# Performance work log

Hardware: AMD Instinct MI355X
Metric: run time of the kernel (lower is better)

Reference implementation:

```python
import jax, jax.numpy as jnp
import numpy as np

B = 65536
IN = 64
H = 128
OUT = 2


def setup_inputs() -> dict:
    key = jax.random.key(0)
    ks = jax.random.split(key, 16)
    s_in = 1.0 / np.sqrt(IN)
    s_h = 1.0 / np.sqrt(H)
    d = {}
    d["x"] = jax.random.normal(ks[0], (B, IN), dtype=jnp.float32)
    # initial state (module resets to zeros per day)
    d["h0"] = jnp.zeros((H,), dtype=jnp.float32)
    d["c0"] = jnp.zeros((B, H), dtype=jnp.float32)
    # input->hidden linears (with bias), torch Linear layout [out, in]
    for i, name in enumerate(["f", "i", "o", "c"]):
        d[f"Wx{name}"] = jax.random.uniform(ks[1 + i], (H, IN), jnp.float32, -s_in, s_in)
        d[f"bx{name}"] = jax.random.uniform(ks[5 + i], (H,), jnp.float32, -s_in, s_in)
        d[f"Wh{name}"] = jax.random.uniform(ks[9 + i], (H, H), jnp.float32, -s_h, s_h)
    d["Wy"] = jax.random.uniform(ks[13], (OUT, H), jnp.float32, -s_h, s_h)
    d["by"] = jax.random.uniform(ks[14], (OUT,), jnp.float32, -s_h, s_h)
    return d


def reference(x, h0, c0, Wxf, bxf, Wxi, bxi, Wxo, bxo, Wxc, bxc, Whf, Whi, Who, Whc, Wy, by):
    # hidden recurrent contributions (h0 is a length-H vector, broadcast over batch)
    hi = h0 @ Whi.T  # [H]
    hf = h0 @ Whf.T
    ho = h0 @ Who.T
    hc = h0 @ Whc.T
    i = jax.nn.sigmoid(x @ Wxi.T + bxi + hi)  # [B, H]
    f = jax.nn.sigmoid(x @ Wxf.T + bxf + hf)
    o = jax.nn.sigmoid(x @ Wxo.T + bxo + ho)
    c_til = jnp.tanh(x @ Wxc.T + bxc + hc)
    c = f * c0 + i * c_til
    h = o * jnp.tanh(c)
    y_hat = h @ Wy.T + by  # [B, OUT]
    return y_hat
```

## Files before the change

### kernel.cpp

```cpp
#include <hip/hip_runtime.h>


#define B_SIZE 65536

typedef __bf16 bf16x8 __attribute__((ext_vector_type(8)));
typedef __bf16 bf16x4 __attribute__((ext_vector_type(4)));
typedef float f32x4 __attribute__((ext_vector_type(4)));

__device__ __forceinline__ float fsig(float x) {
    float e = __builtin_amdgcn_exp2f(-1.442695040888963f * x);
    return __builtin_amdgcn_rcpf(1.0f + e);
}
__device__ __forceinline__ float ftanh(float x) {
    float e = __builtin_amdgcn_exp2f(2.885390081777927f * x);
    return 1.0f - 2.0f * __builtin_amdgcn_rcpf(e + 1.0f);
}

__global__ void bias_kernel(const float* __restrict__ h0,
                            const float* __restrict__ Whf, const float* __restrict__ Whi,
                            const float* __restrict__ Who, const float* __restrict__ Whc,
                            const float* __restrict__ bxf, const float* __restrict__ bxi,
                            const float* __restrict__ bxo, const float* __restrict__ bxc,
                            float* __restrict__ bias512) {
    int j = blockIdx.x * 64 + threadIdx.x;
    int g = j >> 7, r = j & 127;
    const float* Wh = (g == 0) ? Whf : (g == 1) ? Whi : (g == 2) ? Who : Whc;
    const float* bx = (g == 0) ? bxf : (g == 1) ? bxi : (g == 2) ? bxo : bxc;
    float s = bx[r];
    const float4* row = (const float4*)(Wh + r * 128);
    const float4* h4  = (const float4*)h0;
#pragma unroll 8
    for (int k = 0; k < 32; ++k) {
        float4 a = row[k], b = h4[k];
        s += a.x * b.x + a.y * b.y + a.z * b.z + a.w * b.w;
    }
    bias512[j] = s;
}

__launch_bounds__(256, 2)
__global__ void lstm_kernel(const float* __restrict__ x, const float* __restrict__ c0,
                            const float* __restrict__ Wxf, const float* __restrict__ Wxi,
                            const float* __restrict__ Wxo, const float* __restrict__ Wxc,
                            const float* __restrict__ Wy, const float* __restrict__ by,
                            const float* __restrict__ bias512, float* __restrict__ out) {
    __shared__ __bf16 xs[2][1024];
    __shared__ float cs[2][16 * 132];
    __shared__ float yred[4][64][2];

    const int tid  = threadIdx.x;
    const int lane = tid & 63;
    const int w    = tid >> 6;
    const int q    = lane >> 4;
    const int n15  = lane & 15;

    const float* Wxg[4] = {Wxf, Wxi, Wxo, Wxc};
    bf16x8 bw[4][2][2];
    float biasv[4][2];
#pragma unroll
    for (int g = 0; g < 4; ++g) {
#pragma unroll
        for (int cb = 0; cb < 2; ++cb) {
            const int n = w * 32 + cb * 16 + n15;
            biasv[g][cb] = bias512[g * 128 + n];
#pragma unroll
            for (int kb = 0; kb < 2; ++kb) {
                const float* p = Wxg[g] + n * 64 + kb * 32 + q * 8;
                float4 lo = *(const float4*)p;
                float4 hi = *(const float4*)(p + 4);
                bf16x8 v;
                v[0] = (__bf16)lo.x; v[1] = (__bf16)lo.y; v[2] = (__bf16)lo.z; v[3] = (__bf16)lo.w;
                v[4] = (__bf16)hi.x; v[5] = (__bf16)hi.y; v[6] = (__bf16)hi.z; v[7] = (__bf16)hi.w;
                bw[g][cb][kb] = v;
            }
        }
    }
    float wyv[2][2];
#pragma unroll
    for (int o = 0; o < 2; ++o)
#pragma unroll
        for (int cb = 0; cb < 2; ++cb)
            wyv[o][cb] = Wy[o * 128 + w * 32 + cb * 16 + n15];
    const float by0 = by[0], by1 = by[1];

    constexpr int ITERS = (B_SIZE / 16) / 1024;
    const int tile0 = blockIdx.x * ITERS;

    const int xrow = tid >> 4;
    const int k4   = (tid & 15) * 4;
    const int sidx = (k4 >> 5) * 512 + ((k4 & 31) >> 3) * 128 + xrow * 8 + (k4 & 7);

    const int ccol = (tid & 15) * 8;
    const int cidx = xrow * 132 + ccol;

    float4 xr  = *(const float4*)(x  + (size_t)(tile0 * 16 + xrow) * 64 + k4);
    float4 cpa = *(const float4*)(c0 + (size_t)(tile0 * 16 + xrow) * 128 + ccol);
    float4 cpb = *(const float4*)(c0 + (size_t)(tile0 * 16 + xrow) * 128 + ccol + 4);
    {
        bf16x4 v; v[0] = (__bf16)xr.x; v[1] = (__bf16)xr.y; v[2] = (__bf16)xr.z; v[3] = (__bf16)xr.w;
        *(bf16x4*)&xs[0][sidx] = v;
        *(float4*)&cs[0][cidx] = cpa;
        *(float4*)&cs[0][cidx + 4] = cpb;
    }
    xr  = *(const float4*)(x  + (size_t)((tile0 + 1) * 16 + xrow) * 64 + k4);
    cpa = *(const float4*)(c0 + (size_t)((tile0 + 1) * 16 + xrow) * 128 + ccol);
    cpb = *(const float4*)(c0 + (size_t)((tile0 + 1) * 16 + xrow) * 128 + ccol + 4);
    __syncthreads();

#pragma unroll
    for (int it = 0; it < ITERS; ++it) {
        const int cur = it & 1;

        bf16x8 a0 = *(const bf16x8*)&xs[cur][lane * 8];
        bf16x8 a1 = *(const bf16x8*)&xs[cur][512 + lane * 8];

        float c0v[2][4];
#pragma unroll
        for (int cb = 0; cb < 2; ++cb)
#pragma unroll
            for (int r = 0; r < 4; ++r)
                c0v[cb][r] = cs[cur][(q * 4 + r) * 132 + w * 32 + cb * 16 + n15];

        if (it + 1 < ITERS) {
            bf16x4 v; v[0] = (__bf16)xr.x; v[1] = (__bf16)xr.y; v[2] = (__bf16)xr.z; v[3] = (__bf16)xr.w;
            *(bf16x4*)&xs[cur ^ 1][sidx] = v;
            *(float4*)&cs[cur ^ 1][cidx] = cpa;
            *(float4*)&cs[cur ^ 1][cidx + 4] = cpb;
            if (it + 2 < ITERS) {
                const int tn = tile0 + it + 2;
                xr  = *(const float4*)(x  + (size_t)(tn * 16 + xrow) * 64 + k4);
                cpa = *(const float4*)(c0 + (size_t)(tn * 16 + xrow) * 128 + ccol);
                cpb = *(const float4*)(c0 + (size_t)(tn * 16 + xrow) * 128 + ccol + 4);
            }
        }

        f32x4 acc[4][2];
#pragma unroll
        for (int g = 0; g < 4; ++g)
#pragma unroll
            for (int cb = 0; cb < 2; ++cb) {
                float b = biasv[g][cb];
                f32x4 t = {b, b, b, b};
                acc[g][cb] = t;
            }
#pragma unroll
        for (int g = 0; g < 4; ++g)
#pragma unroll
            for (int cb = 0; cb < 2; ++cb) {
                acc[g][cb] = __builtin_amdgcn_mfma_f32_16x16x32_bf16(a0, bw[g][cb][0], acc[g][cb], 0, 0, 0);
                acc[g][cb] = __builtin_amdgcn_mfma_f32_16x16x32_bf16(a1, bw[g][cb][1], acc[g][cb], 0, 0, 0);
            }

        float p0[4] = {0.f, 0.f, 0.f, 0.f};
        float p1[4] = {0.f, 0.f, 0.f, 0.f};
#pragma unroll
        for (int cb = 0; cb < 2; ++cb)
#pragma unroll
            for (int r = 0; r < 4; ++r) {
                float fg = fsig(acc[0][cb][r]);
                float ig = fsig(acc[1][cb][r]);
                float og = fsig(acc[2][cb][r]);
                float ct = ftanh(acc[3][cb][r]);
                float c  = fg * c0v[cb][r] + ig * ct;
                float h  = og * ftanh(c);
                p0[r] += h * wyv[0][cb];
                p1[r] += h * wyv[1][cb];
            }
#pragma unroll
        for (int m = 1; m < 16; m <<= 1) {
#pragma unroll
            for (int r = 0; r < 4; ++r) {
                p0[r] += __shfl_xor(p0[r], m, 64);
                p1[r] += __shfl_xor(p1[r], m, 64);
            }
        }
        if (n15 == 0) {
#pragma unroll
            for (int r = 0; r < 4; ++r) {
                yred[w][it * 16 + q * 4 + r][0] = p0[r];
                yred[w][it * 16 + q * 4 + r][1] = p1[r];
            }
        }
        __syncthreads();
    }

    if (tid < 64) {
        float s0 = by0 + yred[0][tid][0] + yred[1][tid][0] + yred[2][tid][0] + yred[3][tid][0];
        float s1 = by1 + yred[0][tid][1] + yred[1][tid][1] + yred[2][tid][1] + yred[3][tid][1];
        float2 s = {s0, s1};
        *(float2*)(out + (size_t)(tile0 * 16 + tid) * 2) = s;
    }
}

extern "C" void kernel_launch(void* const* d_in, const int* in_sizes, int n_in,
                              void* d_out, int out_size, void* d_ws, size_t ws_size,
                              hipStream_t stream) {
    const float* x   = (const float*)d_in[0];
    const float* h0  = (const float*)d_in[1];
    const float* c0  = (const float*)d_in[2];
    const float* Wxf = (const float*)d_in[3];
    const float* bxf = (const float*)d_in[4];
    const float* Whf = (const float*)d_in[5];
    const float* Wxi = (const float*)d_in[6];
    const float* bxi = (const float*)d_in[7];
    const float* Whi = (const float*)d_in[8];
    const float* Wxo = (const float*)d_in[9];
    const float* bxo = (const float*)d_in[10];
    const float* Who = (const float*)d_in[11];
    const float* Wxc = (const float*)d_in[12];
    const float* bxc = (const float*)d_in[13];
    const float* Whc = (const float*)d_in[14];
    const float* Wy  = (const float*)d_in[15];
    const float* by  = (const float*)d_in[16];
    float* out = (float*)d_out;
    float* bias512 = (float*)d_ws;

    bias_kernel<<<8, 64, 0, stream>>>(h0, Whf, Whi, Who, Whc, bxf, bxi, bxo, bxc, bias512);
    lstm_kernel<<<1024, 256, 0, stream>>>(x, c0, Wxf, Wxi, Wxo, Wxc, Wy, by, bias512, out);
}
```

Baseline: 136.0 us.

## Pre-pack bf16 weight fragments once and halve grid to amortize per-block setup

Adds a prep kernel that converts the four input weight matrices to bf16 MFMA fragment layout once, so each LSTM block loads ready fragments with one vector load instead of two fp32 loads plus conversion. The grid is halved to 512 blocks with 8 tiles each, amortizing weight and bias setup over more batch rows. The cost is an extra kernel launch and fewer blocks in flight, which may reduce latency hiding on a 256-CU device.

```diff
diff --git a/kernel.cpp b/kernel.cpp
--- a/kernel.cpp
+++ b/kernel.cpp
@@ -37,15 +37,34 @@
     bias512[j] = s;
 }
 
+__global__ void prep_kernel(const float* __restrict__ Wxf, const float* __restrict__ Wxi,
+                            const float* __restrict__ Wxo, const float* __restrict__ Wxc,
+                            __bf16* __restrict__ frags) {
+    int t = blockIdx.x * 64 + threadIdx.x;
+    int w    = t >> 10;
+    int g    = (t >> 8) & 3;
+    int cb   = (t >> 7) & 1;
+    int kb   = (t >> 6) & 1;
+    int lane = t & 63;
+    const float* Wx = (g == 0) ? Wxf : (g == 1) ? Wxi : (g == 2) ? Wxo : Wxc;
+    const int n = w * 32 + cb * 16 + (lane & 15);
+    const float* p = Wx + n * 64 + kb * 32 + (lane >> 4) * 8;
+    float4 lo = *(const float4*)p;
+    float4 hi = *(const float4*)(p + 4);
+    bf16x8 v;
+    v[0] = (__bf16)lo.x; v[1] = (__bf16)lo.y; v[2] = (__bf16)lo.z; v[3] = (__bf16)lo.w;
+    v[4] = (__bf16)hi.x; v[5] = (__bf16)hi.y; v[6] = (__bf16)hi.z; v[7] = (__bf16)hi.w;
+    *(bf16x8*)(frags + (size_t)t * 8) = v;
+}
+
 __launch_bounds__(256, 2)
 __global__ void lstm_kernel(const float* __restrict__ x, const float* __restrict__ c0,
-                            const float* __restrict__ Wxf, const float* __restrict__ Wxi,
-                            const float* __restrict__ Wxo, const float* __restrict__ Wxc,
+                            const __bf16* __restrict__ frags,
                             const float* __restrict__ Wy, const float* __restrict__ by,
                             const float* __restrict__ bias512, float* __restrict__ out) {
     __shared__ __bf16 xs[2][1024];
     __shared__ float cs[2][16 * 132];
-    __shared__ float yred[4][64][2];
+    __shared__ float yred[4][128][2];
 
     const int tid  = threadIdx.x;
     const int lane = tid & 63;
@@ -53,27 +72,18 @@
     const int q    = lane >> 4;
     const int n15  = lane & 15;
 
-    const float* Wxg[4] = {Wxf, Wxi, Wxo, Wxc};
     bf16x8 bw[4][2][2];
     float biasv[4][2];
 #pragma unroll
-    for (int g = 0; g < 4; ++g) {
+    for (int g = 0; g < 4; ++g)
 #pragma unroll
         for (int cb = 0; cb < 2; ++cb) {
-            const int n = w * 32 + cb * 16 + n15;
-            biasv[g][cb] = bias512[g * 128 + n];
-#pragma unroll
-            for (int kb = 0; kb < 2; ++kb) {
-                const float* p = Wxg[g] + n * 64 + kb * 32 + q * 8;
-                float4 lo = *(const float4*)p;
-                float4 hi = *(const float4*)(p + 4);
-                bf16x8 v;
-                v[0] = (__bf16)lo.x; v[1] = (__bf16)lo.y; v[2] = (__bf16)lo.z; v[3] = (__bf16)lo.w;
-                v[4] = (__bf16)hi.x; v[5] = (__bf16)hi.y; v[6] = (__bf16)hi.z; v[7] = (__bf16)hi.w;
-                bw[g][cb][kb] = v;
-            }
-        }
-    }
+            biasv[g][cb] = bias512[g * 128 + w * 32 + cb * 16 + n15];
+#pragma unroll
+            for (int kb = 0; kb < 2; ++kb)
+                bw[g][cb][kb] = *(const bf16x8*)(frags +
+                    (size_t)(((w * 16 + g * 4 + cb * 2 + kb) * 64 + lane)) * 8);
+        }
     float wyv[2][2];
 #pragma unroll
     for (int o = 0; o < 2; ++o)
@@ -82,7 +92,7 @@
             wyv[o][cb] = Wy[o * 128 + w * 32 + cb * 16 + n15];
     const float by0 = by[0], by1 = by[1];
 
-    constexpr int ITERS = (B_SIZE / 16) / 1024;
+    constexpr int ITERS = (B_SIZE / 16) / 512;
     const int tile0 = blockIdx.x * ITERS;
 
     const int xrow = tid >> 4;
@@ -183,7 +193,7 @@
         __syncthreads();
     }
 
-    if (tid < 64) {
+    if (tid < 128) {
         float s0 = by0 + yred[0][tid][0] + yred[1][tid][0] + yred[2][tid][0] + yred[3][tid][0];
         float s1 = by1 + yred[0][tid][1] + yred[1][tid][1] + yred[2][tid][1] + yred[3][tid][1];
         float2 s = {s0, s1};
@@ -213,7 +223,9 @@
     const float* by  = (const float*)d_in[16];
     float* out = (float*)d_out;
     float* bias512 = (float*)d_ws;
+    __bf16* frags  = (__bf16*)((float*)d_ws + 512);
 
     bias_kernel<<<8, 64, 0, stream>>>(h0, Whf, Whi, Who, Whc, bxf, bxi, bxo, bxc, bias512);
-    lstm_kernel<<<1024, 256, 0, stream>>>(x, c0, Wxf, Wxi, Wxo, Wxc, Wy, by, bias512, out);
-}
+    prep_kernel<<<64, 64, 0, stream>>>(Wxf, Wxi, Wxo, Wxc, frags);
+    lstm_kernel<<<512, 256, 0, stream>>>(x, c0, frags, Wy, by, bias512, out);
+}
```

Measured after the change: 126.1 us. -7.2%, faster.
